# Performance work log

Hardware: AMD Instinct MI355X
Metric: run time of the kernel (lower is better)

The kernel has to match this reference:

```python
import jax, jax.numpy as jnp
import numpy as np

B, T, C, H = 4, 2048, 1024, 16


def setup_inputs() -> dict:
    key = jax.random.key(0)
    ks = jax.random.split(key, 5)
    s_attn = 1.0 / np.sqrt(C)
    s_proj = 1.0 / np.sqrt(C)
    return {
        "x": jax.random.normal(ks[0], (B, T, C), dtype=jnp.float32),
        "w_attn": jax.random.uniform(ks[1], (3 * C, C), dtype=jnp.float32, minval=-s_attn, maxval=s_attn),
        "b_attn": jax.random.uniform(ks[2], (3 * C,), dtype=jnp.float32, minval=-s_attn, maxval=s_attn),
        "w_proj": jax.random.uniform(ks[3], (C, C), dtype=jnp.float32, minval=-s_proj, maxval=s_proj),
        "b_proj": jax.random.uniform(ks[4], (C,), dtype=jnp.float32, minval=-s_proj, maxval=s_proj),
    }


def reference(x, w_attn, b_attn, w_proj, b_proj):
    b, t, c = x.shape
    hd = c // H  # head dim
    qkv = jnp.einsum('btc,dc->btd', x, w_attn) + b_attn  # [B,T,3C]
    q, k, v = jnp.split(qkv, 3, axis=-1)
    # [B,H,T,hd]
    q = q.reshape(b, t, H, hd).transpose(0, 2, 1, 3)
    k = k.reshape(b, t, H, hd).transpose(0, 2, 1, 3)
    v = v.reshape(b, t, H, hd).transpose(0, 2, 1, 3)
    att = jnp.einsum('bhqd,bhkd->bhqk', q, k) * (1.0 / np.sqrt(hd))
    mask = jnp.tril(jnp.ones((t, t), dtype=bool))  # causal
    att = jnp.where(mask, att, -jnp.inf)
    att = jax.nn.softmax(att, axis=-1)
    y = jnp.einsum('bhqk,bhkd->bhqd', att, v)
    y = y.transpose(0, 2, 1, 3).reshape(b, t, c)
    return jnp.einsum('btc,dc->btd', y, w_proj) + b_proj
```

## Files before the change

kernel.cpp:

```cpp
#include <hip/hip_runtime.h>

#define Bb 4
#define Tt 2048
#define Cc 1024
#define Hh 16
#define NQKV 3072
#define Mtot 8192

typedef __bf16 bf16_t;
typedef unsigned short u16;
typedef __bf16 bf16x8 __attribute__((ext_vector_type(8)));
typedef __bf16 bf16x4 __attribute__((ext_vector_type(4)));
typedef short short4v __attribute__((ext_vector_type(4)));
typedef float f32x4 __attribute__((ext_vector_type(4)));
typedef float f32x16 __attribute__((ext_vector_type(16)));
typedef unsigned uint2v __attribute__((ext_vector_type(2)));

union bfu { bf16_t b; u16 u; };
union trpair { short4v h[2]; bf16x8 v; };
union pfu { unsigned u[4]; bf16x8 v; };

#define QSCALE 0.18033688011112042f

#define TRD(dst, addr, OFF)                                                     \
  asm volatile("ds_read_b64_tr_b16 %0, %1 offset:" OFF                          \
               : "=v"(dst) : "v"(addr) : "memory")

__device__ __forceinline__ unsigned cvtpk(float a, float b) {
  unsigned r;
  asm("v_cvt_pk_bf16_f32 %0, %1, %2" : "=v"(r) : "v"(a), "v"(b));
  return r;
}
__device__ __forceinline__ uint2v plswap(unsigned a, unsigned b) {
  return __builtin_amdgcn_permlane32_swap(a, b, false, false);
}

__global__ __launch_bounds__(256) void cvt_f32_bf16(const float* __restrict__ s,
                                                    u16* __restrict__ d,
                                                    long nscale, float factor) {
  size_t i = ((size_t)blockIdx.x * 256 + threadIdx.x) * 8;
  const float f = ((long)i < nscale) ? factor : 1.0f;
  float4 a = *(const float4*)(s + i);
  float4 b = *(const float4*)(s + i + 4);
  bf16x8 v;
  v[0]=(bf16_t)(a.x*f); v[1]=(bf16_t)(a.y*f); v[2]=(bf16_t)(a.z*f); v[3]=(bf16_t)(a.w*f);
  v[4]=(bf16_t)(b.x*f); v[5]=(bf16_t)(b.y*f); v[6]=(bf16_t)(b.z*f); v[7]=(bf16_t)(b.w*f);
  *(bf16x8*)(d + i) = v;
}

__global__ __launch_bounds__(256) void scale_bias(const float* __restrict__ s,
                                                  float* __restrict__ d) {
  int i = blockIdx.x * 256 + threadIdx.x;
  d[i] = s[i] * ((i < Cc) ? QSCALE : 1.0f);
}

template <int OUTBF16>
__global__ __launch_bounds__(256) void gemm_bf16(
    const u16* __restrict__ A, const u16* __restrict__ Bm,
    const float* __restrict__ bias, void* __restrict__ Cout,
    int M, int N, int K)
{
  __shared__ __attribute__((aligned(16))) u16 sa[128][40];
  __shared__ __attribute__((aligned(16))) u16 sb[128][40];

  const int tid  = threadIdx.x;
  const int lane = tid & 63;
  const int wid  = tid >> 6;
  const int wr   = (wid >> 1) * 64;
  const int wc   = (wid & 1) * 64;
  const int l15  = lane & 15;
  const int lh   = lane >> 4;
  const int bm   = blockIdx.x * 128;
  const int bn   = blockIdx.y * 128;

  f32x4 acc[4][4] = {};

  const int srow = tid >> 1;
  const int sseg = (tid & 1) * 16;

  const u16* pa = A  + (size_t)(bm + srow) * K + sseg;
  const u16* pb = Bm + (size_t)(bn + srow) * K + sseg;

  uint4 ar0 = *(const uint4*)pa, ar1 = *(const uint4*)(pa + 8);
  uint4 br0 = *(const uint4*)pb, br1 = *(const uint4*)(pb + 8);
  pa += 32; pb += 32;

  for (int k0 = 0; k0 < K; k0 += 32) {
    __syncthreads();
    *(uint4*)&sa[srow][sseg]     = ar0;
    *(uint4*)&sa[srow][sseg + 8] = ar1;
    *(uint4*)&sb[srow][sseg]     = br0;
    *(uint4*)&sb[srow][sseg + 8] = br1;
    __syncthreads();
    if (k0 + 32 < K) {
      ar0 = *(const uint4*)pa; ar1 = *(const uint4*)(pa + 8);
      br0 = *(const uint4*)pb; br1 = *(const uint4*)(pb + 8);
      pa += 32; pb += 32;
    }
    bf16x8 af[4], bfv[4];
#pragma unroll
    for (int mi = 0; mi < 4; mi++)
      af[mi] = *(const bf16x8*)&sa[wr + mi*16 + l15][lh * 8];
#pragma unroll
    for (int ni = 0; ni < 4; ni++)
      bfv[ni] = *(const bf16x8*)&sb[wc + ni*16 + l15][lh * 8];
#pragma unroll
    for (int mi = 0; mi < 4; mi++)
#pragma unroll
      for (int ni = 0; ni < 4; ni++)
        acc[mi][ni] = __builtin_amdgcn_mfma_f32_16x16x32_bf16(
            af[mi], bfv[ni], acc[mi][ni], 0, 0, 0);
  }

#pragma unroll
  for (int mi = 0; mi < 4; mi++) {
#pragma unroll
    for (int ni = 0; ni < 4; ni++) {
      const int col = bn + wc + ni*16 + l15;
      const float bs = bias[col];
#pragma unroll
      for (int r = 0; r < 4; r++) {
        const int row = bm + wr + mi*16 + lh*4 + r;
        const float val = acc[mi][ni][r] + bs;
        if (OUTBF16) {
          bfu cv; cv.b = (bf16_t)val;
          ((u16*)Cout)[(size_t)row * N + col] = cv.u;
        } else {
          ((float*)Cout)[(size_t)row * N + col] = val;
        }
      }
    }
  }
}

#define V0u 4608
__global__ __launch_bounds__(256) void attn_kernel(
    const u16* __restrict__ qkv, u16* __restrict__ y)
{
  __shared__ __attribute__((aligned(16))) u16 smem[9216];

  const int tid  = threadIdx.x;
  const int lane = tid & 63;
  const int w    = tid >> 6;
  const int l31  = lane & 31;
  const int hh   = lane >> 5;
  const int l15  = lane & 15;
  const int lh   = lane >> 4;
  const int bh   = blockIdx.y;
  const int b    = bh >> 4;
  const int head = bh & 15;

  const size_t rowbase = (size_t)b * Tt * NQKV;

  const int skey = tid >> 2;
  const int sp   = tid & 3;
  const u16* kbase = qkv + rowbase + 1024 + head*64 + sp*16;
  const u16* vbase = qkv + rowbase + 2048 + head*64 + sp*16;

  const unsigned smemB = (unsigned)(size_t)(&smem[0]);
  const unsigned vaddr = smemB + 2*V0u
      + ((lh>>1)*8 + (l15>>2))*144 + (lh&1)*32 + (l15&3)*8;

  for (int half = 0; half < 2; ++half) {
    const int qb    = half ? (15 - (int)blockIdx.x) : (int)blockIdx.x;
    const int qbase = qb * 128;
    const int qw    = qbase + w * 32;
    const int qi    = qw + l31;
    const int ktiles = 2*qb + 2;

    bf16x8 qfrag[4];
#pragma unroll
    for (int m = 0; m < 4; ++m)
      qfrag[m] = *(const bf16x8*)(qkv + rowbase + (size_t)qi * NQKV
                                  + head*64 + m*16 + hh*8);

    f32x16 o0 = {}, o1 = {};
    float m_run = -1e30f, l_part = 0.0f;

    uint4 kr0 = *(const uint4*)(kbase + (size_t)skey * NQKV);
    uint4 kr1 = *(const uint4*)(kbase + (size_t)skey * NQKV + 8);
    uint4 vr0 = *(const uint4*)(vbase + (size_t)skey * NQKV);
    uint4 vr1 = *(const uint4*)(vbase + (size_t)skey * NQKV + 8);

    for (int kt = 0; kt < ktiles; ++kt) {
      __syncthreads();
      *(uint4*)&smem[skey*72 + sp*16]           = kr0;
      *(uint4*)&smem[skey*72 + sp*16 + 8]       = kr1;
      *(uint4*)&smem[V0u + skey*72 + sp*16]     = vr0;
      *(uint4*)&smem[V0u + skey*72 + sp*16 + 8] = vr1;
      __syncthreads();

      if (kt + 1 < ktiles) {
        const u16* kp = kbase + (size_t)((kt+1)*64 + skey) * NQKV;
        const u16* vp = vbase + (size_t)((kt+1)*64 + skey) * NQKV;
        kr0 = *(const uint4*)kp; kr1 = *(const uint4*)(kp + 8);
        vr0 = *(const uint4*)vp; vr1 = *(const uint4*)(vp + 8);
      }

      if (kt*64 <= qw + 31) {
        f32x16 s0 = {}, s1 = {};
#pragma unroll
        for (int m = 0; m < 4; ++m) {
          bf16x8 k0 = *(const bf16x8*)&smem[(l31)*72      + m*16 + hh*8];
          bf16x8 k1 = *(const bf16x8*)&smem[(32 + l31)*72 + m*16 + hh*8];
          s0 = __builtin_amdgcn_mfma_f32_32x32x16_bf16(k0, qfrag[m], s0, 0,0,0);
          s1 = __builtin_amdgcn_mfma_f32_32x32x16_bf16(k1, qfrag[m], s1, 0,0,0);
        }

        if (kt*64 + 63 > qw) {
          const int kb0 = kt*64;
#pragma unroll
          for (int r = 0; r < 16; ++r) {
            const int crow = (r&3) + 8*(r>>2) + 4*hh;
            if (kb0 + crow > qi)      s0[r] = -1e30f;
            if (kb0 + 32 + crow > qi) s1[r] = -1e30f;
          }
        }

        float rm = s0[0];
#pragma unroll
        for (int r = 1; r < 16; ++r) rm = fmaxf(rm, s0[r]);
#pragma unroll
        for (int r = 0; r < 16; ++r) rm = fmaxf(rm, s1[r]);
        {
          uint2v t = plswap(__float_as_uint(rm), __float_as_uint(rm));
          rm = fmaxf(__uint_as_float(t[0]), __uint_as_float(t[1]));
        }
        if (__any(rm > m_run + 8.0f)) {
          const float mn = fmaxf(m_run, rm);
          const float al = exp2f(m_run - mn);
          m_run = mn; l_part *= al;
#pragma unroll
          for (int r = 0; r < 16; ++r) { o0[r] *= al; o1[r] *= al; }
        }

        pfu pf0, pf1, pf2, pf3;
        {
          float pe[16];
#pragma unroll
          for (int r = 0; r < 16; ++r) { pe[r] = exp2f(s0[r] - m_run); l_part += pe[r]; }
          unsigned a0 = cvtpk(pe[0],pe[1]),  a1 = cvtpk(pe[2],pe[3]);
          unsigned a2 = cvtpk(pe[4],pe[5]),  a3 = cvtpk(pe[6],pe[7]);
          uint2v x1 = plswap(a0, a2), x2 = plswap(a1, a3);
          pf0.u[0]=x1[0]; pf0.u[1]=x2[0]; pf0.u[2]=x1[1]; pf0.u[3]=x2[1];
          unsigned b0 = cvtpk(pe[8],pe[9]),  b1 = cvtpk(pe[10],pe[11]);
          unsigned b2 = cvtpk(pe[12],pe[13]), b3 = cvtpk(pe[14],pe[15]);
          uint2v x3 = plswap(b0, b2), x4 = plswap(b1, b3);
          pf1.u[0]=x3[0]; pf1.u[1]=x4[0]; pf1.u[2]=x3[1]; pf1.u[3]=x4[1];
        }
        {
          float pe[16];
#pragma unroll
          for (int r = 0; r < 16; ++r) { pe[r] = exp2f(s1[r] - m_run); l_part += pe[r]; }
          unsigned a0 = cvtpk(pe[0],pe[1]),  a1 = cvtpk(pe[2],pe[3]);
          unsigned a2 = cvtpk(pe[4],pe[5]),  a3 = cvtpk(pe[6],pe[7]);
          uint2v x1 = plswap(a0, a2), x2 = plswap(a1, a3);
          pf2.u[0]=x1[0]; pf2.u[1]=x2[0]; pf2.u[2]=x1[1]; pf2.u[3]=x2[1];
          unsigned b0 = cvtpk(pe[8],pe[9]),  b1 = cvtpk(pe[10],pe[11]);
          unsigned b2 = cvtpk(pe[12],pe[13]), b3 = cvtpk(pe[14],pe[15]);
          uint2v x3 = plswap(b0, b2), x4 = plswap(b1, b3);
          pf3.u[0]=x3[0]; pf3.u[1]=x4[0]; pf3.u[2]=x3[1]; pf3.u[3]=x4[1];
        }

        short4v ta0,tb0,ta1,tb1,ta2,tb2,ta3,tb3,ta4,tb4,ta5,tb5,ta6,tb6,ta7,tb7;
        TRD(ta0, vaddr, "0");    TRD(tb0, vaddr, "576");
        TRD(ta1, vaddr, "64");   TRD(tb1, vaddr, "640");
        TRD(ta2, vaddr, "2304"); TRD(tb2, vaddr, "2880");
        TRD(ta3, vaddr, "2368"); TRD(tb3, vaddr, "2944");
        TRD(ta4, vaddr, "4608"); TRD(tb4, vaddr, "5184");
        TRD(ta5, vaddr, "4672"); TRD(tb5, vaddr, "5248");
        TRD(ta6, vaddr, "6912"); TRD(tb6, vaddr, "7488");
        TRD(ta7, vaddr, "6976"); TRD(tb7, vaddr, "7552");
        asm volatile("s_waitcnt lgkmcnt(0)" ::: "memory");
        __builtin_amdgcn_sched_barrier(0);
        trpair v00,v01,v10,v11,v20,v21,v30,v31;
        v00.h[0]=ta0; v00.h[1]=tb0;  v01.h[0]=ta1; v01.h[1]=tb1;
        v10.h[0]=ta2; v10.h[1]=tb2;  v11.h[0]=ta3; v11.h[1]=tb3;
        v20.h[0]=ta4; v20.h[1]=tb4;  v21.h[0]=ta5; v21.h[1]=tb5;
        v30.h[0]=ta6; v30.h[1]=tb6;  v31.h[0]=ta7; v31.h[1]=tb7;
        o0 = __builtin_amdgcn_mfma_f32_32x32x16_bf16(v00.v, pf0.v, o0, 0,0,0);
        o1 = __builtin_amdgcn_mfma_f32_32x32x16_bf16(v01.v, pf0.v, o1, 0,0,0);
        o0 = __builtin_amdgcn_mfma_f32_32x32x16_bf16(v10.v, pf1.v, o0, 0,0,0);
        o1 = __builtin_amdgcn_mfma_f32_32x32x16_bf16(v11.v, pf1.v, o1, 0,0,0);
        o0 = __builtin_amdgcn_mfma_f32_32x32x16_bf16(v20.v, pf2.v, o0, 0,0,0);
        o1 = __builtin_amdgcn_mfma_f32_32x32x16_bf16(v21.v, pf2.v, o1, 0,0,0);
        o0 = __builtin_amdgcn_mfma_f32_32x32x16_bf16(v30.v, pf3.v, o0, 0,0,0);
        o1 = __builtin_amdgcn_mfma_f32_32x32x16_bf16(v31.v, pf3.v, o1, 0,0,0);
      }
    }

    {
      uint2v t = plswap(__float_as_uint(l_part), __float_as_uint(l_part));
      l_part = __uint_as_float(t[0]) + __uint_as_float(t[1]);
    }
    const float inv = 1.0f / l_part;

    __syncthreads();
#pragma unroll
    for (int k4 = 0; k4 < 4; ++k4) {
      bf16x4 pa, pb;
#pragma unroll
      for (int j = 0; j < 4; ++j) {
        pa[j] = (bf16_t)(o0[4*k4 + j] * inv);
        pb[j] = (bf16_t)(o1[4*k4 + j] * inv);
      }
      *(bf16x4*)&smem[w*2304 + l31*72 +      8*k4 + 4*hh] = pa;
      *(bf16x4*)&smem[w*2304 + l31*72 + 32 + 8*k4 + 4*hh] = pb;
    }
    u16* yp = y + ((size_t)(b*Tt + qi)) * Cc + head*64;
#pragma unroll
    for (int p = 0; p < 4; ++p) {
      bf16x8 row = *(const bf16x8*)&smem[w*2304 + l31*72 + p*16 + hh*8];
      *(bf16x8*)(yp + p*16 + hh*8) = row;
    }
  }
}

extern "C" void kernel_launch(void* const* d_in, const int* in_sizes, int n_in,
                              void* d_out, int out_size, void* d_ws, size_t ws_size,
                              hipStream_t stream) {
  const float* x      = (const float*)d_in[0];
  const float* w_attn = (const float*)d_in[1];
  const float* b_attn = (const float*)d_in[2];
  const float* w_proj = (const float*)d_in[3];
  const float* b_proj = (const float*)d_in[4];
  float* out = (float*)d_out;

  char* ws = (char*)d_ws;
  u16*   xb    = (u16*)(ws + 0);
  u16*   wab   = (u16*)(ws + 16777216);
  u16*   wpb   = (u16*)(ws + 23068672);
  u16*   qkvb  = (u16*)(ws + 25165824);
  u16*   yb    = (u16*)(ws + 75497472);
  float* sbias = (float*)(ws + 92274688);

  cvt_f32_bf16<<<4096, 256, 0, stream>>>(x,      xb,  0, 1.0f);
  cvt_f32_bf16<<<1536, 256, 0, stream>>>(w_attn, wab, (long)Cc*Cc, QSCALE);
  cvt_f32_bf16<<<512,  256, 0, stream>>>(w_proj, wpb, 0, 1.0f);
  scale_bias<<<12, 256, 0, stream>>>(b_attn, sbias);

  gemm_bf16<1><<<dim3(Mtot/128, NQKV/128), 256, 0, stream>>>(
      xb, wab, sbias, (void*)qkvb, Mtot, NQKV, Cc);

  attn_kernel<<<dim3(8, Bb*Hh), 256, 0, stream>>>(qkvb, yb);

  gemm_bf16<0><<<dim3(Mtot/128, Cc/128), 256, 0, stream>>>(
      yb, wpb, b_proj, (void*)out, Mtot, Cc, Cc);
}
```

Before: 192.3 us.

## Use direct global-to-LDS loads in GEMM and split attention into one q-block per workgroup

The GEMM's tile staging changes from register-held prefetch plus LDS stores to global_load_lds direct copies into an unpadded 32-column LDS layout. This drops the register round trip, but it also drops the register-level prefetch overlap and the row padding, so LDS bank conflicts may rise. The attention kernel no longer pairs two query blocks (qb and 15-qb) per workgroup. It launches 16 workgroups per head, each handling a single q-block in reverse order so the heaviest blocks start first, which adds parallelism at the cost of less balanced per-workgroup work.

```diff
diff --git a/kernel.cpp b/kernel.cpp
--- a/kernel.cpp
+++ b/kernel.cpp
@@ -34,6 +34,11 @@
 __device__ __forceinline__ uint2v plswap(unsigned a, unsigned b) {
   return __builtin_amdgcn_permlane32_swap(a, b, false, false);
 }
+
+#define GLOAD16(gsrc, ldst)                                                     \
+  __builtin_amdgcn_global_load_lds(                                             \
+      (const __attribute__((address_space(1))) unsigned int*)(gsrc),            \
+      (__attribute__((address_space(3))) unsigned int*)(ldst), 16, 0, 0)
 
 __global__ __launch_bounds__(256) void cvt_f32_bf16(const float* __restrict__ s,
                                                     u16* __restrict__ d,
@@ -60,8 +65,8 @@
     const float* __restrict__ bias, void* __restrict__ Cout,
     int M, int N, int K)
 {
-  __shared__ __attribute__((aligned(16))) u16 sa[128][40];
-  __shared__ __attribute__((aligned(16))) u16 sb[128][40];
+  __shared__ __attribute__((aligned(16))) u16 sa[128 * 32];
+  __shared__ __attribute__((aligned(16))) u16 sb[128 * 32];
 
   const int tid  = threadIdx.x;
   const int lane = tid & 63;
@@ -75,35 +80,32 @@
 
   f32x4 acc[4][4] = {};
 
-  const int srow = tid >> 1;
-  const int sseg = (tid & 1) * 16;
-
-  const u16* pa = A  + (size_t)(bm + srow) * K + sseg;
-  const u16* pb = Bm + (size_t)(bn + srow) * K + sseg;
-
-  uint4 ar0 = *(const uint4*)pa, ar1 = *(const uint4*)(pa + 8);
-  uint4 br0 = *(const uint4*)pb, br1 = *(const uint4*)(pb + 8);
-  pa += 32; pb += 32;
+  const int r0 = wid * 32 + (lane >> 2);
+  const int c0 = (lane & 3) * 8;
+  const u16* pa0 = A  + (size_t)(bm + r0) * K + c0;
+  const u16* pb0 = Bm + (size_t)(bn + r0) * K + c0;
+  u16* sA0 = sa + wid * 1024;
+  u16* sA1 = sa + wid * 1024 + 512;
+  u16* sB0 = sb + wid * 1024;
+  u16* sB1 = sb + wid * 1024 + 512;
+  const size_t k16 = (size_t)16 * K;
 
   for (int k0 = 0; k0 < K; k0 += 32) {
     __syncthreads();
-    *(uint4*)&sa[srow][sseg]     = ar0;
-    *(uint4*)&sa[srow][sseg + 8] = ar1;
-    *(uint4*)&sb[srow][sseg]     = br0;
-    *(uint4*)&sb[srow][sseg + 8] = br1;
+    GLOAD16(pa0,       sA0);
+    GLOAD16(pa0 + k16, sA1);
+    GLOAD16(pb0,       sB0);
+    GLOAD16(pb0 + k16, sB1);
+    pa0 += 32; pb0 += 32;
     __syncthreads();
-    if (k0 + 32 < K) {
-      ar0 = *(const uint4*)pa; ar1 = *(const uint4*)(pa + 8);
-      br0 = *(const uint4*)pb; br1 = *(const uint4*)(pb + 8);
-      pa += 32; pb += 32;
-    }
+
     bf16x8 af[4], bfv[4];
 #pragma unroll
     for (int mi = 0; mi < 4; mi++)
-      af[mi] = *(const bf16x8*)&sa[wr + mi*16 + l15][lh * 8];
+      af[mi] = *(const bf16x8*)&sa[(wr + mi*16 + l15) * 32 + lh * 8];
 #pragma unroll
     for (int ni = 0; ni < 4; ni++)
-      bfv[ni] = *(const bf16x8*)&sb[wc + ni*16 + l15][lh * 8];
+      bfv[ni] = *(const bf16x8*)&sb[(wc + ni*16 + l15) * 32 + lh * 8];
 #pragma unroll
     for (int mi = 0; mi < 4; mi++)
 #pragma unroll
@@ -161,158 +163,156 @@
   const unsigned vaddr = smemB + 2*V0u
       + ((lh>>1)*8 + (l15>>2))*144 + (lh&1)*32 + (l15&3)*8;
 
-  for (int half = 0; half < 2; ++half) {
-    const int qb    = half ? (15 - (int)blockIdx.x) : (int)blockIdx.x;
-    const int qbase = qb * 128;
-    const int qw    = qbase + w * 32;
-    const int qi    = qw + l31;
-    const int ktiles = 2*qb + 2;
-
-    bf16x8 qfrag[4];
-#pragma unroll
-    for (int m = 0; m < 4; ++m)
-      qfrag[m] = *(const bf16x8*)(qkv + rowbase + (size_t)qi * NQKV
-                                  + head*64 + m*16 + hh*8);
-
-    f32x16 o0 = {}, o1 = {};
-    float m_run = -1e30f, l_part = 0.0f;
-
-    uint4 kr0 = *(const uint4*)(kbase + (size_t)skey * NQKV);
-    uint4 kr1 = *(const uint4*)(kbase + (size_t)skey * NQKV + 8);
-    uint4 vr0 = *(const uint4*)(vbase + (size_t)skey * NQKV);
-    uint4 vr1 = *(const uint4*)(vbase + (size_t)skey * NQKV + 8);
-
-    for (int kt = 0; kt < ktiles; ++kt) {
-      __syncthreads();
-      *(uint4*)&smem[skey*72 + sp*16]           = kr0;
-      *(uint4*)&smem[skey*72 + sp*16 + 8]       = kr1;
-      *(uint4*)&smem[V0u + skey*72 + sp*16]     = vr0;
-      *(uint4*)&smem[V0u + skey*72 + sp*16 + 8] = vr1;
-      __syncthreads();
-
-      if (kt + 1 < ktiles) {
-        const u16* kp = kbase + (size_t)((kt+1)*64 + skey) * NQKV;
-        const u16* vp = vbase + (size_t)((kt+1)*64 + skey) * NQKV;
-        kr0 = *(const uint4*)kp; kr1 = *(const uint4*)(kp + 8);
-        vr0 = *(const uint4*)vp; vr1 = *(const uint4*)(vp + 8);
-      }
-
-      if (kt*64 <= qw + 31) {
-        f32x16 s0 = {}, s1 = {};
-#pragma unroll
-        for (int m = 0; m < 4; ++m) {
-          bf16x8 k0 = *(const bf16x8*)&smem[(l31)*72      + m*16 + hh*8];
-          bf16x8 k1 = *(const bf16x8*)&smem[(32 + l31)*72 + m*16 + hh*8];
-          s0 = __builtin_amdgcn_mfma_f32_32x32x16_bf16(k0, qfrag[m], s0, 0,0,0);
-          s1 = __builtin_amdgcn_mfma_f32_32x32x16_bf16(k1, qfrag[m], s1, 0,0,0);
+  const int qb    = 15 - (int)blockIdx.x;
+  const int qbase = qb * 128;
+  const int qw    = qbase + w * 32;
+  const int qi    = qw + l31;
+  const int ktiles = 2*qb + 2;
+
+  bf16x8 qfrag[4];
+#pragma unroll
+  for (int m = 0; m < 4; ++m)
+    qfrag[m] = *(const bf16x8*)(qkv + rowbase + (size_t)qi * NQKV
+                                + head*64 + m*16 + hh*8);
+
+  f32x16 o0 = {}, o1 = {};
+  float m_run = -1e30f, l_part = 0.0f;
+
+  uint4 kr0 = *(const uint4*)(kbase + (size_t)skey * NQKV);
+  uint4 kr1 = *(const uint4*)(kbase + (size_t)skey * NQKV + 8);
+  uint4 vr0 = *(const uint4*)(vbase + (size_t)skey * NQKV);
+  uint4 vr1 = *(const uint4*)(vbase + (size_t)skey * NQKV + 8);
+
+  for (int kt = 0; kt < ktiles; ++kt) {
+    __syncthreads();
+    *(uint4*)&smem[skey*72 + sp*16]           = kr0;
+    *(uint4*)&smem[skey*72 + sp*16 + 8]       = kr1;
+    *(uint4*)&smem[V0u + skey*72 + sp*16]     = vr0;
+    *(uint4*)&smem[V0u + skey*72 + sp*16 + 8] = vr1;
+    __syncthreads();
+
+    if (kt + 1 < ktiles) {
+      const u16* kp = kbase + (size_t)((kt+1)*64 + skey) * NQKV;
+      const u16* vp = vbase + (size_t)((kt+1)*64 + skey) * NQKV;
+      kr0 = *(const uint4*)kp; kr1 = *(const uint4*)(kp + 8);
+      vr0 = *(const uint4*)vp; vr1 = *(const uint4*)(vp + 8);
+    }
+
+    if (kt*64 <= qw + 31) {
+      f32x16 s0 = {}, s1 = {};
+#pragma unroll
+      for (int m = 0; m < 4; ++m) {
+        bf16x8 k0 = *(const bf16x8*)&smem[(l31)*72      + m*16 + hh*8];
+        bf16x8 k1 = *(const bf16x8*)&smem[(32 + l31)*72 + m*16 + hh*8];
+        s0 = __builtin_amdgcn_mfma_f32_32x32x16_bf16(k0, qfrag[m], s0, 0,0,0);
+        s1 = __builtin_amdgcn_mfma_f32_32x32x16_bf16(k1, qfrag[m], s1, 0,0,0);
+      }
+
+      if (kt*64 + 63 > qw) {
+        const int kb0 = kt*64;
+#pragma unroll
+        for (int r = 0; r < 16; ++r) {
+          const int crow = (r&3) + 8*(r>>2) + 4*hh;
+          if (kb0 + crow > qi)      s0[r] = -1e30f;
+          if (kb0 + 32 + crow > qi) s1[r] = -1e30f;
         }
-
-        if (kt*64 + 63 > qw) {
-          const int kb0 = kt*64;
-#pragma unroll
-          for (int r = 0; r < 16; ++r) {
-            const int crow = (r&3) + 8*(r>>2) + 4*hh;
-            if (kb0 + crow > qi)      s0[r] = -1e30f;
-            if (kb0 + 32 + crow > qi) s1[r] = -1e30f;
-          }
-        }
-
-        float rm = s0[0];
-#pragma unroll
-        for (int r = 1; r < 16; ++r) rm = fmaxf(rm, s0[r]);
-#pragma unroll
-        for (int r = 0; r < 16; ++r) rm = fmaxf(rm, s1[r]);
-        {
-          uint2v t = plswap(__float_as_uint(rm), __float_as_uint(rm));
-          rm = fmaxf(__uint_as_float(t[0]), __uint_as_float(t[1]));
-        }
-        if (__any(rm > m_run + 8.0f)) {
-          const float mn = fmaxf(m_run, rm);
-          const float al = exp2f(m_run - mn);
-          m_run = mn; l_part *= al;
-#pragma unroll
-          for (int r = 0; r < 16; ++r) { o0[r] *= al; o1[r] *= al; }
-        }
-
-        pfu pf0, pf1, pf2, pf3;
-        {
-          float pe[16];
-#pragma unroll
-          for (int r = 0; r < 16; ++r) { pe[r] = exp2f(s0[r] - m_run); l_part += pe[r]; }
-          unsigned a0 = cvtpk(pe[0],pe[1]),  a1 = cvtpk(pe[2],pe[3]);
-          unsigned a2 = cvtpk(pe[4],pe[5]),  a3 = cvtpk(pe[6],pe[7]);
-          uint2v x1 = plswap(a0, a2), x2 = plswap(a1, a3);
-          pf0.u[0]=x1[0]; pf0.u[1]=x2[0]; pf0.u[2]=x1[1]; pf0.u[3]=x2[1];
-          unsigned b0 = cvtpk(pe[8],pe[9]),  b1 = cvtpk(pe[10],pe[11]);
-          unsigned b2 = cvtpk(pe[12],pe[13]), b3 = cvtpk(pe[14],pe[15]);
-          uint2v x3 = plswap(b0, b2), x4 = plswap(b1, b3);
-          pf1.u[0]=x3[0]; pf1.u[1]=x4[0]; pf1.u[2]=x3[1]; pf1.u[3]=x4[1];
-        }
-        {
-          float pe[16];
-#pragma unroll
-          for (int r = 0; r < 16; ++r) { pe[r] = exp2f(s1[r] - m_run); l_part += pe[r]; }
-          unsigned a0 = cvtpk(pe[0],pe[1]),  a1 = cvtpk(pe[2],pe[3]);
-          unsigned a2 = cvtpk(pe[4],pe[5]),  a3 = cvtpk(pe[6],pe[7]);
-          uint2v x1 = plswap(a0, a2), x2 = plswap(a1, a3);
-          pf2.u[0]=x1[0]; pf2.u[1]=x2[0]; pf2.u[2]=x1[1]; pf2.u[3]=x2[1];
-          unsigned b0 = cvtpk(pe[8],pe[9]),  b1 = cvtpk(pe[10],pe[11]);
-          unsigned b2 = cvtpk(pe[12],pe[13]), b3 = cvtpk(pe[14],pe[15]);
-          uint2v x3 = plswap(b0, b2), x4 = plswap(b1, b3);
-          pf3.u[0]=x3[0]; pf3.u[1]=x4[0]; pf3.u[2]=x3[1]; pf3.u[3]=x4[1];
-        }
-
-        short4v ta0,tb0,ta1,tb1,ta2,tb2,ta3,tb3,ta4,tb4,ta5,tb5,ta6,tb6,ta7,tb7;
-        TRD(ta0, vaddr, "0");    TRD(tb0, vaddr, "576");
-        TRD(ta1, vaddr, "64");   TRD(tb1, vaddr, "640");
-        TRD(ta2, vaddr, "2304"); TRD(tb2, vaddr, "2880");
-        TRD(ta3, vaddr, "2368"); TRD(tb3, vaddr, "2944");
-        TRD(ta4, vaddr, "4608"); TRD(tb4, vaddr, "5184");
-        TRD(ta5, vaddr, "4672"); TRD(tb5, vaddr, "5248");
-        TRD(ta6, vaddr, "6912"); TRD(tb6, vaddr, "7488");
-        TRD(ta7, vaddr, "6976"); TRD(tb7, vaddr, "7552");
-        asm volatile("s_waitcnt lgkmcnt(0)" ::: "memory");
-        __builtin_amdgcn_sched_barrier(0);
-        trpair v00,v01,v10,v11,v20,v21,v30,v31;
-        v00.h[0]=ta0; v00.h[1]=tb0;  v01.h[0]=ta1; v01.h[1]=tb1;
-        v10.h[0]=ta2; v10.h[1]=tb2;  v11.h[0]=ta3; v11.h[1]=tb3;
-        v20.h[0]=ta4; v20.h[1]=tb4;  v21.h[0]=ta5; v21.h[1]=tb5;
-        v30.h[0]=ta6; v30.h[1]=tb6;  v31.h[0]=ta7; v31.h[1]=tb7;
-        o0 = __builtin_amdgcn_mfma_f32_32x32x16_bf16(v00.v, pf0.v, o0, 0,0,0);
-        o1 = __builtin_amdgcn_mfma_f32_32x32x16_bf16(v01.v, pf0.v, o1, 0,0,0);
-        o0 = __builtin_amdgcn_mfma_f32_32x32x16_bf16(v10.v, pf1.v, o0, 0,0,0);
-        o1 = __builtin_amdgcn_mfma_f32_32x32x16_bf16(v11.v, pf1.v, o1, 0,0,0);
-        o0 = __builtin_amdgcn_mfma_f32_32x32x16_bf16(v20.v, pf2.v, o0, 0,0,0);
-        o1 = __builtin_amdgcn_mfma_f32_32x32x16_bf16(v21.v, pf2.v, o1, 0,0,0);
-        o0 = __builtin_amdgcn_mfma_f32_32x32x16_bf16(v30.v, pf3.v, o0, 0,0,0);
-        o1 = __builtin_amdgcn_mfma_f32_32x32x16_bf16(v31.v, pf3.v, o1, 0,0,0);
-      }
+      }
+
+      float rm = s0[0];
+#pragma unroll
+      for (int r = 1; r < 16; ++r) rm = fmaxf(rm, s0[r]);
+#pragma unroll
+      for (int r = 0; r < 16; ++r) rm = fmaxf(rm, s1[r]);
+      {
+        uint2v t = plswap(__float_as_uint(rm), __float_as_uint(rm));
+        rm = fmaxf(__uint_as_float(t[0]), __uint_as_float(t[1]));
+      }
+      if (__any(rm > m_run + 8.0f)) {
+        const float mn = fmaxf(m_run, rm);
+        const float al = exp2f(m_run - mn);
+        m_run = mn; l_part *= al;
+#pragma unroll
+        for (int r = 0; r < 16; ++r) { o0[r] *= al; o1[r] *= al; }
+      }
+
+      pfu pf0, pf1, pf2, pf3;
+      {
+        float pe[16];
+#pragma unroll
+        for (int r = 0; r < 16; ++r) { pe[r] = exp2f(s0[r] - m_run); l_part += pe[r]; }
+        unsigned a0 = cvtpk(pe[0],pe[1]),  a1 = cvtpk(pe[2],pe[3]);
+        unsigned a2 = cvtpk(pe[4],pe[5]),  a3 = cvtpk(pe[6],pe[7]);
+        uint2v x1 = plswap(a0, a2), x2 = plswap(a1, a3);
+        pf0.u[0]=x1[0]; pf0.u[1]=x2[0]; pf0.u[2]=x1[1]; pf0.u[3]=x2[1];
+        unsigned b0 = cvtpk(pe[8],pe[9]),  b1 = cvtpk(pe[10],pe[11]);
+        unsigned b2 = cvtpk(pe[12],pe[13]), b3 = cvtpk(pe[14],pe[15]);
+        uint2v x3 = plswap(b0, b2), x4 = plswap(b1, b3);
+        pf1.u[0]=x3[0]; pf1.u[1]=x4[0]; pf1.u[2]=x3[1]; pf1.u[3]=x4[1];
+      }
+      {
+        float pe[16];
+#pragma unroll
+        for (int r = 0; r < 16; ++r) { pe[r] = exp2f(s1[r] - m_run); l_part += pe[r]; }
+        unsigned a0 = cvtpk(pe[0],pe[1]),  a1 = cvtpk(pe[2],pe[3]);
+        unsigned a2 = cvtpk(pe[4],pe[5]),  a3 = cvtpk(pe[6],pe[7]);
+        uint2v x1 = plswap(a0, a2), x2 = plswap(a1, a3);
+        pf2.u[0]=x1[0]; pf2.u[1]=x2[0]; pf2.u[2]=x1[1]; pf2.u[3]=x2[1];
+        unsigned b0 = cvtpk(pe[8],pe[9]),  b1 = cvtpk(pe[10],pe[11]);
+        unsigned b2 = cvtpk(pe[12],pe[13]), b3 = cvtpk(pe[14],pe[15]);
+        uint2v x3 = plswap(b0, b2), x4 = plswap(b1, b3);
+        pf3.u[0]=x3[0]; pf3.u[1]=x4[0]; pf3.u[2]=x3[1]; pf3.u[3]=x4[1];
+      }
+
+      short4v ta0,tb0,ta1,tb1,ta2,tb2,ta3,tb3,ta4,tb4,ta5,tb5,ta6,tb6,ta7,tb7;
+      TRD(ta0, vaddr, "0");    TRD(tb0, vaddr, "576");
+      TRD(ta1, vaddr, "64");   TRD(tb1, vaddr, "640");
+      TRD(ta2, vaddr, "2304"); TRD(tb2, vaddr, "2880");
+      TRD(ta3, vaddr, "2368"); TRD(tb3, vaddr, "2944");
+      TRD(ta4, vaddr, "4608"); TRD(tb4, vaddr, "5184");
+      TRD(ta5, vaddr, "4672"); TRD(tb5, vaddr, "5248");
+      TRD(ta6, vaddr, "6912"); TRD(tb6, vaddr, "7488");
+      TRD(ta7, vaddr, "6976"); TRD(tb7, vaddr, "7552");
+      asm volatile("s_waitcnt lgkmcnt(0)" ::: "memory");
+      __builtin_amdgcn_sched_barrier(0);
+      trpair v00,v01,v10,v11,v20,v21,v30,v31;
+      v00.h[0]=ta0; v00.h[1]=tb0;  v01.h[0]=ta1; v01.h[1]=tb1;
+      v10.h[0]=ta2; v10.h[1]=tb2;  v11.h[0]=ta3; v11.h[1]=tb3;
+      v20.h[0]=ta4; v20.h[1]=tb4;  v21.h[0]=ta5; v21.h[1]=tb5;
+      v30.h[0]=ta6; v30.h[1]=tb6;  v31.h[0]=ta7; v31.h[1]=tb7;
+      o0 = __builtin_amdgcn_mfma_f32_32x32x16_bf16(v00.v, pf0.v, o0, 0,0,0);
+      o1 = __builtin_amdgcn_mfma_f32_32x32x16_bf16(v01.v, pf0.v, o1, 0,0,0);
+      o0 = __builtin_amdgcn_mfma_f32_32x32x16_bf16(v10.v, pf1.v, o0, 0,0,0);
+      o1 = __builtin_amdgcn_mfma_f32_32x32x16_bf16(v11.v, pf1.v, o1, 0,0,0);
+      o0 = __builtin_amdgcn_mfma_f32_32x32x16_bf16(v20.v, pf2.v, o0, 0,0,0);
+      o1 = __builtin_amdgcn_mfma_f32_32x32x16_bf16(v21.v, pf2.v, o1, 0,0,0);
+      o0 = __builtin_amdgcn_mfma_f32_32x32x16_bf16(v30.v, pf3.v, o0, 0,0,0);
+      o1 = __builtin_amdgcn_mfma_f32_32x32x16_bf16(v31.v, pf3.v, o1, 0,0,0);
     }
-
-    {
-      uint2v t = plswap(__float_as_uint(l_part), __float_as_uint(l_part));
-      l_part = __uint_as_float(t[0]) + __uint_as_float(t[1]);
+  }
+
+  {
+    uint2v t = plswap(__float_as_uint(l_part), __float_as_uint(l_part));
+    l_part = __uint_as_float(t[0]) + __uint_as_float(t[1]);
+  }
+  const float inv = 1.0f / l_part;
+
+  __syncthreads();
+#pragma unroll
+  for (int k4 = 0; k4 < 4; ++k4) {
+    bf16x4 pa, pb;
+#pragma unroll
+    for (int j = 0; j < 4; ++j) {
+      pa[j] = (bf16_t)(o0[4*k4 + j] * inv);
+      pb[j] = (bf16_t)(o1[4*k4 + j] * inv);
     }
-    const float inv = 1.0f / l_part;
-
-    __syncthreads();
-#pragma unroll
-    for (int k4 = 0; k4 < 4; ++k4) {
-      bf16x4 pa, pb;
-#pragma unroll
-      for (int j = 0; j < 4; ++j) {
-        pa[j] = (bf16_t)(o0[4*k4 + j] * inv);
-        pb[j] = (bf16_t)(o1[4*k4 + j] * inv);
-      }
-      *(bf16x4*)&smem[w*2304 + l31*72 +      8*k4 + 4*hh] = pa;
-      *(bf16x4*)&smem[w*2304 + l31*72 + 32 + 8*k4 + 4*hh] = pb;
-    }
-    u16* yp = y + ((size_t)(b*Tt + qi)) * Cc + head*64;
-#pragma unroll
-    for (int p = 0; p < 4; ++p) {
-      bf16x8 row = *(const bf16x8*)&smem[w*2304 + l31*72 + p*16 + hh*8];
-      *(bf16x8*)(yp + p*16 + hh*8) = row;
-    }
+    *(bf16x4*)&smem[w*2304 + l31*72 +      8*k4 + 4*hh] = pa;
+    *(bf16x4*)&smem[w*2304 + l31*72 + 32 + 8*k4 + 4*hh] = pb;
+  }
+  u16* yp = y + ((size_t)(b*Tt + qi)) * Cc + head*64;
+#pragma unroll
+  for (int p = 0; p < 4; ++p) {
+    bf16x8 row = *(const bf16x8*)&smem[w*2304 + l31*72 + p*16 + hh*8];
+    *(bf16x8*)(yp + p*16 + hh*8) = row;
   }
 }
 
@@ -342,7 +342,7 @@
   gemm_bf16<1><<<dim3(Mtot/128, NQKV/128), 256, 0, stream>>>(
       xb, wab, sbias, (void*)qkvb, Mtot, NQKV, Cc);
 
-  attn_kernel<<<dim3(8, Bb*Hh), 256, 0, stream>>>(qkvb, yb);
+  attn_kernel<<<dim3(16, Bb*Hh), 256, 0, stream>>>(qkvb, yb);
 
   gemm_bf16<0><<<dim3(Mtot/128, Cc/128), 256, 0, stream>>>(
       yb, wpb, b_proj, (void*)out, Mtot, Cc, Cc);
```

After: 249.8 us. 1.3x slower.

## Double attention key tile to 128 keys and pipeline PV in sections

Applied to the files above, without the earlier changes.

The attention kernel now stages 128 keys per iteration instead of 64, with shared memory doubled and each thread loading 32-element K/V chunks. This halves the number of block-wide barriers and global-to-shared staging rounds per query block, and the row-max reduction becomes a tree. The PV product is split into four macro sections, each interleaving its transposed V loads with the exp/convert work for one score block, so LDS reads overlap ALU work. The cost is more registers and LDS, lower occupancy, and more work wasted on masked keys: the per-warp causal skip is gone, so waves whose rows lie entirely before the tile's upper half still compute it.

```diff
diff --git a/kernel.cpp b/kernel.cpp
--- a/kernel.cpp
+++ b/kernel.cpp
@@ -133,11 +133,42 @@
   }
 }
 
-#define V0u 4608
+#define VBYTE 18432
+
+#define PVSEC(SV, A0,A1,A2,A3, A4,A5,A6,A7) do {                                \
+  short4v t0,t1,t2,t3,t4,t5,t6,t7;                                              \
+  TRD(t0, vaddr, A0); TRD(t1, vaddr, A1); TRD(t2, vaddr, A2);                   \
+  TRD(t3, vaddr, A3); TRD(t4, vaddr, A4); TRD(t5, vaddr, A5);                   \
+  TRD(t6, vaddr, A6); TRD(t7, vaddr, A7);                                       \
+  pfu pfa, pfb;                                                                 \
+  {                                                                             \
+    float pe[16];                                                               \
+    _Pragma("unroll")                                                           \
+    for (int r = 0; r < 16; ++r) { pe[r] = exp2f(SV[r] - m_run); l_part += pe[r]; } \
+    unsigned a0=cvtpk(pe[0],pe[1]),   a1=cvtpk(pe[2],pe[3]);                    \
+    unsigned a2=cvtpk(pe[4],pe[5]),   a3=cvtpk(pe[6],pe[7]);                    \
+    uint2v x1=plswap(a0,a2), x2=plswap(a1,a3);                                  \
+    pfa.u[0]=x1[0]; pfa.u[1]=x2[0]; pfa.u[2]=x1[1]; pfa.u[3]=x2[1];             \
+    unsigned b0=cvtpk(pe[8],pe[9]),   b1=cvtpk(pe[10],pe[11]);                  \
+    unsigned b2=cvtpk(pe[12],pe[13]), b3=cvtpk(pe[14],pe[15]);                  \
+    uint2v x3=plswap(b0,b2), x4=plswap(b1,b3);                                  \
+    pfb.u[0]=x3[0]; pfb.u[1]=x4[0]; pfb.u[2]=x3[1]; pfb.u[3]=x4[1];             \
+  }                                                                             \
+  asm volatile("s_waitcnt lgkmcnt(0)" ::: "memory");                            \
+  __builtin_amdgcn_sched_barrier(0);                                            \
+  trpair va,vb,vc,vd;                                                           \
+  va.h[0]=t0; va.h[1]=t1;  vb.h[0]=t2; vb.h[1]=t3;                              \
+  vc.h[0]=t4; vc.h[1]=t5;  vd.h[0]=t6; vd.h[1]=t7;                              \
+  o0 = __builtin_amdgcn_mfma_f32_32x32x16_bf16(va.v, pfa.v, o0, 0,0,0);         \
+  o1 = __builtin_amdgcn_mfma_f32_32x32x16_bf16(vb.v, pfa.v, o1, 0,0,0);         \
+  o0 = __builtin_amdgcn_mfma_f32_32x32x16_bf16(vc.v, pfb.v, o0, 0,0,0);         \
+  o1 = __builtin_amdgcn_mfma_f32_32x32x16_bf16(vd.v, pfb.v, o1, 0,0,0);         \
+} while (0)
+
 __global__ __launch_bounds__(256) void attn_kernel(
     const u16* __restrict__ qkv, u16* __restrict__ y)
 {
-  __shared__ __attribute__((aligned(16))) u16 smem[9216];
+  __shared__ __attribute__((aligned(16))) u16 smem[18432];
 
   const int tid  = threadIdx.x;
   const int lane = tid & 63;
@@ -152,13 +183,13 @@
 
   const size_t rowbase = (size_t)b * Tt * NQKV;
 
-  const int skey = tid >> 2;
-  const int sp   = tid & 3;
-  const u16* kbase = qkv + rowbase + 1024 + head*64 + sp*16;
-  const u16* vbase = qkv + rowbase + 2048 + head*64 + sp*16;
+  const int skey = tid >> 1;
+  const int sp   = tid & 1;
+  const u16* kbase = qkv + rowbase + 1024 + head*64 + sp*32;
+  const u16* vbase = qkv + rowbase + 2048 + head*64 + sp*32;
 
   const unsigned smemB = (unsigned)(size_t)(&smem[0]);
-  const unsigned vaddr = smemB + 2*V0u
+  const unsigned vaddr = smemB + VBYTE
       + ((lh>>1)*8 + (l15>>2))*144 + (lh&1)*32 + (l15&3)*8;
 
   for (int half = 0; half < 2; ++half) {
@@ -166,7 +197,7 @@
     const int qbase = qb * 128;
     const int qw    = qbase + w * 32;
     const int qi    = qw + l31;
-    const int ktiles = 2*qb + 2;
+    const int ktiles = qb + 1;
 
     bf16x8 qfrag[4];
 #pragma unroll
@@ -177,116 +208,90 @@
     f32x16 o0 = {}, o1 = {};
     float m_run = -1e30f, l_part = 0.0f;
 
-    uint4 kr0 = *(const uint4*)(kbase + (size_t)skey * NQKV);
-    uint4 kr1 = *(const uint4*)(kbase + (size_t)skey * NQKV + 8);
-    uint4 vr0 = *(const uint4*)(vbase + (size_t)skey * NQKV);
-    uint4 vr1 = *(const uint4*)(vbase + (size_t)skey * NQKV + 8);
+    uint4 kr0, kr1, kr2, kr3, vr0, vr1, vr2, vr3;
+    {
+      const u16* kp = kbase + (size_t)skey * NQKV;
+      const u16* vp = vbase + (size_t)skey * NQKV;
+      kr0 = ((const uint4*)kp)[0]; kr1 = ((const uint4*)kp)[1];
+      kr2 = ((const uint4*)kp)[2]; kr3 = ((const uint4*)kp)[3];
+      vr0 = ((const uint4*)vp)[0]; vr1 = ((const uint4*)vp)[1];
+      vr2 = ((const uint4*)vp)[2]; vr3 = ((const uint4*)vp)[3];
+    }
 
     for (int kt = 0; kt < ktiles; ++kt) {
       __syncthreads();
-      *(uint4*)&smem[skey*72 + sp*16]           = kr0;
-      *(uint4*)&smem[skey*72 + sp*16 + 8]       = kr1;
-      *(uint4*)&smem[V0u + skey*72 + sp*16]     = vr0;
-      *(uint4*)&smem[V0u + skey*72 + sp*16 + 8] = vr1;
+      {
+        u16* dK = &smem[skey*72 + sp*32];
+        *(uint4*)dK        = kr0; *(uint4*)(dK + 8)  = kr1;
+        *(uint4*)(dK + 16) = kr2; *(uint4*)(dK + 24) = kr3;
+        u16* dV = dK + 9216;
+        *(uint4*)dV        = vr0; *(uint4*)(dV + 8)  = vr1;
+        *(uint4*)(dV + 16) = vr2; *(uint4*)(dV + 24) = vr3;
+      }
       __syncthreads();
 
       if (kt + 1 < ktiles) {
-        const u16* kp = kbase + (size_t)((kt+1)*64 + skey) * NQKV;
-        const u16* vp = vbase + (size_t)((kt+1)*64 + skey) * NQKV;
-        kr0 = *(const uint4*)kp; kr1 = *(const uint4*)(kp + 8);
-        vr0 = *(const uint4*)vp; vr1 = *(const uint4*)(vp + 8);
-      }
-
-      if (kt*64 <= qw + 31) {
-        f32x16 s0 = {}, s1 = {};
-#pragma unroll
-        for (int m = 0; m < 4; ++m) {
-          bf16x8 k0 = *(const bf16x8*)&smem[(l31)*72      + m*16 + hh*8];
-          bf16x8 k1 = *(const bf16x8*)&smem[(32 + l31)*72 + m*16 + hh*8];
-          s0 = __builtin_amdgcn_mfma_f32_32x32x16_bf16(k0, qfrag[m], s0, 0,0,0);
-          s1 = __builtin_amdgcn_mfma_f32_32x32x16_bf16(k1, qfrag[m], s1, 0,0,0);
+        const u16* kp = kbase + (size_t)((kt+1)*128 + skey) * NQKV;
+        const u16* vp = vbase + (size_t)((kt+1)*128 + skey) * NQKV;
+        kr0 = ((const uint4*)kp)[0]; kr1 = ((const uint4*)kp)[1];
+        kr2 = ((const uint4*)kp)[2]; kr3 = ((const uint4*)kp)[3];
+        vr0 = ((const uint4*)vp)[0]; vr1 = ((const uint4*)vp)[1];
+        vr2 = ((const uint4*)vp)[2]; vr3 = ((const uint4*)vp)[3];
+      }
+
+      f32x16 s0 = {}, s1 = {}, s2 = {}, s3 = {};
+#pragma unroll
+      for (int m = 0; m < 4; ++m) {
+        const int co = m*16 + hh*8;
+        bf16x8 k0 = *(const bf16x8*)&smem[(l31)*72      + co];
+        bf16x8 k1 = *(const bf16x8*)&smem[(32 + l31)*72 + co];
+        bf16x8 k2 = *(const bf16x8*)&smem[(64 + l31)*72 + co];
+        bf16x8 k3 = *(const bf16x8*)&smem[(96 + l31)*72 + co];
+        s0 = __builtin_amdgcn_mfma_f32_32x32x16_bf16(k0, qfrag[m], s0, 0,0,0);
+        s1 = __builtin_amdgcn_mfma_f32_32x32x16_bf16(k1, qfrag[m], s1, 0,0,0);
+        s2 = __builtin_amdgcn_mfma_f32_32x32x16_bf16(k2, qfrag[m], s2, 0,0,0);
+        s3 = __builtin_amdgcn_mfma_f32_32x32x16_bf16(k3, qfrag[m], s3, 0,0,0);
+      }
+
+      if (kt*128 + 127 > qw) {
+        const int kb0 = kt*128;
+#pragma unroll
+        for (int r = 0; r < 16; ++r) {
+          const int crow = (r&3) + 8*(r>>2) + 4*hh;
+          if (kb0 + crow > qi)      s0[r] = -1e30f;
+          if (kb0 + 32 + crow > qi) s1[r] = -1e30f;
+          if (kb0 + 64 + crow > qi) s2[r] = -1e30f;
+          if (kb0 + 96 + crow > qi) s3[r] = -1e30f;
         }
-
-        if (kt*64 + 63 > qw) {
-          const int kb0 = kt*64;
-#pragma unroll
-          for (int r = 0; r < 16; ++r) {
-            const int crow = (r&3) + 8*(r>>2) + 4*hh;
-            if (kb0 + crow > qi)      s0[r] = -1e30f;
-            if (kb0 + 32 + crow > qi) s1[r] = -1e30f;
-          }
-        }
-
-        float rm = s0[0];
-#pragma unroll
-        for (int r = 1; r < 16; ++r) rm = fmaxf(rm, s0[r]);
-#pragma unroll
-        for (int r = 0; r < 16; ++r) rm = fmaxf(rm, s1[r]);
-        {
-          uint2v t = plswap(__float_as_uint(rm), __float_as_uint(rm));
-          rm = fmaxf(__uint_as_float(t[0]), __uint_as_float(t[1]));
-        }
-        if (__any(rm > m_run + 8.0f)) {
-          const float mn = fmaxf(m_run, rm);
-          const float al = exp2f(m_run - mn);
-          m_run = mn; l_part *= al;
-#pragma unroll
-          for (int r = 0; r < 16; ++r) { o0[r] *= al; o1[r] *= al; }
-        }
-
-        pfu pf0, pf1, pf2, pf3;
-        {
-          float pe[16];
-#pragma unroll
-          for (int r = 0; r < 16; ++r) { pe[r] = exp2f(s0[r] - m_run); l_part += pe[r]; }
-          unsigned a0 = cvtpk(pe[0],pe[1]),  a1 = cvtpk(pe[2],pe[3]);
-          unsigned a2 = cvtpk(pe[4],pe[5]),  a3 = cvtpk(pe[6],pe[7]);
-          uint2v x1 = plswap(a0, a2), x2 = plswap(a1, a3);
-          pf0.u[0]=x1[0]; pf0.u[1]=x2[0]; pf0.u[2]=x1[1]; pf0.u[3]=x2[1];
-          unsigned b0 = cvtpk(pe[8],pe[9]),  b1 = cvtpk(pe[10],pe[11]);
-          unsigned b2 = cvtpk(pe[12],pe[13]), b3 = cvtpk(pe[14],pe[15]);
-          uint2v x3 = plswap(b0, b2), x4 = plswap(b1, b3);
-          pf1.u[0]=x3[0]; pf1.u[1]=x4[0]; pf1.u[2]=x3[1]; pf1.u[3]=x4[1];
-        }
-        {
-          float pe[16];
-#pragma unroll
-          for (int r = 0; r < 16; ++r) { pe[r] = exp2f(s1[r] - m_run); l_part += pe[r]; }
-          unsigned a0 = cvtpk(pe[0],pe[1]),  a1 = cvtpk(pe[2],pe[3]);
-          unsigned a2 = cvtpk(pe[4],pe[5]),  a3 = cvtpk(pe[6],pe[7]);
-          uint2v x1 = plswap(a0, a2), x2 = plswap(a1, a3);
-          pf2.u[0]=x1[0]; pf2.u[1]=x2[0]; pf2.u[2]=x1[1]; pf2.u[3]=x2[1];
-          unsigned b0 = cvtpk(pe[8],pe[9]),  b1 = cvtpk(pe[10],pe[11]);
-          unsigned b2 = cvtpk(pe[12],pe[13]), b3 = cvtpk(pe[14],pe[15]);
-          uint2v x3 = plswap(b0, b2), x4 = plswap(b1, b3);
-          pf3.u[0]=x3[0]; pf3.u[1]=x4[0]; pf3.u[2]=x3[1]; pf3.u[3]=x4[1];
-        }
-
-        short4v ta0,tb0,ta1,tb1,ta2,tb2,ta3,tb3,ta4,tb4,ta5,tb5,ta6,tb6,ta7,tb7;
-        TRD(ta0, vaddr, "0");    TRD(tb0, vaddr, "576");
-        TRD(ta1, vaddr, "64");   TRD(tb1, vaddr, "640");
-        TRD(ta2, vaddr, "2304"); TRD(tb2, vaddr, "2880");
-        TRD(ta3, vaddr, "2368"); TRD(tb3, vaddr, "2944");
-        TRD(ta4, vaddr, "4608"); TRD(tb4, vaddr, "5184");
-        TRD(ta5, vaddr, "4672"); TRD(tb5, vaddr, "5248");
-        TRD(ta6, vaddr, "6912"); TRD(tb6, vaddr, "7488");
-        TRD(ta7, vaddr, "6976"); TRD(tb7, vaddr, "7552");
-        asm volatile("s_waitcnt lgkmcnt(0)" ::: "memory");
-        __builtin_amdgcn_sched_barrier(0);
-        trpair v00,v01,v10,v11,v20,v21,v30,v31;
-        v00.h[0]=ta0; v00.h[1]=tb0;  v01.h[0]=ta1; v01.h[1]=tb1;
-        v10.h[0]=ta2; v10.h[1]=tb2;  v11.h[0]=ta3; v11.h[1]=tb3;
-        v20.h[0]=ta4; v20.h[1]=tb4;  v21.h[0]=ta5; v21.h[1]=tb5;
-        v30.h[0]=ta6; v30.h[1]=tb6;  v31.h[0]=ta7; v31.h[1]=tb7;
-        o0 = __builtin_amdgcn_mfma_f32_32x32x16_bf16(v00.v, pf0.v, o0, 0,0,0);
-        o1 = __builtin_amdgcn_mfma_f32_32x32x16_bf16(v01.v, pf0.v, o1, 0,0,0);
-        o0 = __builtin_amdgcn_mfma_f32_32x32x16_bf16(v10.v, pf1.v, o0, 0,0,0);
-        o1 = __builtin_amdgcn_mfma_f32_32x32x16_bf16(v11.v, pf1.v, o1, 0,0,0);
-        o0 = __builtin_amdgcn_mfma_f32_32x32x16_bf16(v20.v, pf2.v, o0, 0,0,0);
-        o1 = __builtin_amdgcn_mfma_f32_32x32x16_bf16(v21.v, pf2.v, o1, 0,0,0);
-        o0 = __builtin_amdgcn_mfma_f32_32x32x16_bf16(v30.v, pf3.v, o0, 0,0,0);
-        o1 = __builtin_amdgcn_mfma_f32_32x32x16_bf16(v31.v, pf3.v, o1, 0,0,0);
-      }
+      }
+
+      float ma[16];
+#pragma unroll
+      for (int r = 0; r < 16; ++r)
+        ma[r] = fmaxf(fmaxf(s0[r], s1[r]), fmaxf(s2[r], s3[r]));
+      float t8[8], t4[4], t2[2];
+#pragma unroll
+      for (int i = 0; i < 8; ++i) t8[i] = fmaxf(ma[i], ma[i+8]);
+#pragma unroll
+      for (int i = 0; i < 4; ++i) t4[i] = fmaxf(t8[i], t8[i+4]);
+      t2[0] = fmaxf(t4[0], t4[2]); t2[1] = fmaxf(t4[1], t4[3]);
+      float rm = fmaxf(t2[0], t2[1]);
+      {
+        uint2v t = plswap(__float_as_uint(rm), __float_as_uint(rm));
+        rm = fmaxf(__uint_as_float(t[0]), __uint_as_float(t[1]));
+      }
+      if (__any(rm > m_run + 8.0f)) {
+        const float mn = fmaxf(m_run, rm);
+        const float al = exp2f(m_run - mn);
+        m_run = mn; l_part *= al;
+#pragma unroll
+        for (int r = 0; r < 16; ++r) { o0[r] *= al; o1[r] *= al; }
+      }
+
+      PVSEC(s0, "0","576","64","640",          "2304","2880","2368","2944");
+      PVSEC(s1, "4608","5184","4672","5248",   "6912","7488","6976","7552");
+      PVSEC(s2, "9216","9792","9280","9856",   "11520","12096","11584","12160");
+      PVSEC(s3, "13824","14400","13888","14464","16128","16704","16192","16768");
     }
 
     {
```

Result: slower. 220.7 us (+14.8%).

## Split attention key range across two wave groups with in-block softmax merge

Applied to the files above, without the earlier changes.

The attention block grows from 256 to 512 threads. Two groups of four waves each process alternating 64-key halves of a 128-key tile for the same 128 queries, which halves the serial key-tile loop per wave. At the end, group 1 writes its running max, sum and partial O into shared memory, and group 0 merges them with the rescaled online-softmax combine before normalizing and storing. This adds parallelism per (batch, head) block and uses twice the LDS, at the cost of a merge step, extra barriers, and higher register and LDS pressure per CU.

```diff
diff --git a/kernel.cpp b/kernel.cpp
--- a/kernel.cpp
+++ b/kernel.cpp
@@ -19,6 +19,7 @@
 union bfu { bf16_t b; u16 u; };
 union trpair { short4v h[2]; bf16x8 v; };
 union pfu { unsigned u[4]; bf16x8 v; };
+union o16 { f32x16 v; f32x4 q[4]; };
 
 #define QSCALE 0.18033688011112042f
 
@@ -133,15 +134,16 @@
   }
 }
 
-#define V0u 4608
-__global__ __launch_bounds__(256) void attn_kernel(
+__global__ __launch_bounds__(512, 4) void attn_kernel(
     const u16* __restrict__ qkv, u16* __restrict__ y)
 {
-  __shared__ __attribute__((aligned(16))) u16 smem[9216];
+  __shared__ __attribute__((aligned(16))) u16 smem[18432];
 
   const int tid  = threadIdx.x;
   const int lane = tid & 63;
   const int w    = tid >> 6;
+  const int hw   = w >> 2;
+  const int ch   = w & 3;
   const int l31  = lane & 31;
   const int hh   = lane >> 5;
   const int l15  = lane & 15;
@@ -158,15 +160,15 @@
   const u16* vbase = qkv + rowbase + 2048 + head*64 + sp*16;
 
   const unsigned smemB = (unsigned)(size_t)(&smem[0]);
-  const unsigned vaddr = smemB + 2*V0u
+  const unsigned vaddr = smemB + 18432 + hw*9216
       + ((lh>>1)*8 + (l15>>2))*144 + (lh&1)*32 + (l15&3)*8;
 
   for (int half = 0; half < 2; ++half) {
     const int qb    = half ? (15 - (int)blockIdx.x) : (int)blockIdx.x;
     const int qbase = qb * 128;
-    const int qw    = qbase + w * 32;
+    const int qw    = qbase + ch * 32;
     const int qi    = qw + l31;
-    const int ktiles = 2*qb + 2;
+    const int ktiles = qb + 1;
 
     bf16x8 qfrag[4];
 #pragma unroll
@@ -177,43 +179,47 @@
     f32x16 o0 = {}, o1 = {};
     float m_run = -1e30f, l_part = 0.0f;
 
-    uint4 kr0 = *(const uint4*)(kbase + (size_t)skey * NQKV);
-    uint4 kr1 = *(const uint4*)(kbase + (size_t)skey * NQKV + 8);
-    uint4 vr0 = *(const uint4*)(vbase + (size_t)skey * NQKV);
-    uint4 vr1 = *(const uint4*)(vbase + (size_t)skey * NQKV + 8);
+    uint4 kr0, kr1, vr0, vr1;
+    {
+      const u16* kp = kbase + (size_t)skey * NQKV;
+      const u16* vp = vbase + (size_t)skey * NQKV;
+      kr0 = ((const uint4*)kp)[0]; kr1 = ((const uint4*)kp)[1];
+      vr0 = ((const uint4*)vp)[0]; vr1 = ((const uint4*)vp)[1];
+    }
 
     for (int kt = 0; kt < ktiles; ++kt) {
       __syncthreads();
-      *(uint4*)&smem[skey*72 + sp*16]           = kr0;
-      *(uint4*)&smem[skey*72 + sp*16 + 8]       = kr1;
-      *(uint4*)&smem[V0u + skey*72 + sp*16]     = vr0;
-      *(uint4*)&smem[V0u + skey*72 + sp*16 + 8] = vr1;
+      *(uint4*)&smem[skey*72 + sp*16]          = kr0;
+      *(uint4*)&smem[skey*72 + sp*16 + 8]      = kr1;
+      *(uint4*)&smem[9216 + skey*72 + sp*16]   = vr0;
+      *(uint4*)&smem[9216 + skey*72 + sp*16+8] = vr1;
       __syncthreads();
 
       if (kt + 1 < ktiles) {
-        const u16* kp = kbase + (size_t)((kt+1)*64 + skey) * NQKV;
-        const u16* vp = vbase + (size_t)((kt+1)*64 + skey) * NQKV;
-        kr0 = *(const uint4*)kp; kr1 = *(const uint4*)(kp + 8);
-        vr0 = *(const uint4*)vp; vr1 = *(const uint4*)(vp + 8);
-      }
-
-      if (kt*64 <= qw + 31) {
+        const u16* kp = kbase + (size_t)((kt+1)*128 + skey) * NQKV;
+        const u16* vp = vbase + (size_t)((kt+1)*128 + skey) * NQKV;
+        kr0 = ((const uint4*)kp)[0]; kr1 = ((const uint4*)kp)[1];
+        vr0 = ((const uint4*)vp)[0]; vr1 = ((const uint4*)vp)[1];
+      }
+
+      const int keyw = kt*128 + hw*64;
+      if (keyw <= qw + 31) {
         f32x16 s0 = {}, s1 = {};
 #pragma unroll
         for (int m = 0; m < 4; ++m) {
-          bf16x8 k0 = *(const bf16x8*)&smem[(l31)*72      + m*16 + hh*8];
-          bf16x8 k1 = *(const bf16x8*)&smem[(32 + l31)*72 + m*16 + hh*8];
+          const int co = m*16 + hh*8;
+          bf16x8 k0 = *(const bf16x8*)&smem[(hw*64 +      l31)*72 + co];
+          bf16x8 k1 = *(const bf16x8*)&smem[(hw*64 + 32 + l31)*72 + co];
           s0 = __builtin_amdgcn_mfma_f32_32x32x16_bf16(k0, qfrag[m], s0, 0,0,0);
           s1 = __builtin_amdgcn_mfma_f32_32x32x16_bf16(k1, qfrag[m], s1, 0,0,0);
         }
 
-        if (kt*64 + 63 > qw) {
-          const int kb0 = kt*64;
+        if (keyw + 63 > qw) {
 #pragma unroll
           for (int r = 0; r < 16; ++r) {
             const int crow = (r&3) + 8*(r>>2) + 4*hh;
-            if (kb0 + crow > qi)      s0[r] = -1e30f;
-            if (kb0 + 32 + crow > qi) s1[r] = -1e30f;
+            if (keyw + crow > qi)      s0[r] = -1e30f;
+            if (keyw + 32 + crow > qi) s1[r] = -1e30f;
           }
         }
 
@@ -289,29 +295,58 @@
       }
     }
 
-    {
-      uint2v t = plswap(__float_as_uint(l_part), __float_as_uint(l_part));
-      l_part = __uint_as_float(t[0]) + __uint_as_float(t[1]);
-    }
-    const float inv = 1.0f / l_part;
-
     __syncthreads();
-#pragma unroll
-    for (int k4 = 0; k4 < 4; ++k4) {
-      bf16x4 pa, pb;
-#pragma unroll
-      for (int j = 0; j < 4; ++j) {
-        pa[j] = (bf16_t)(o0[4*k4 + j] * inv);
-        pb[j] = (bf16_t)(o1[4*k4 + j] * inv);
-      }
-      *(bf16x4*)&smem[w*2304 + l31*72 +      8*k4 + 4*hh] = pa;
-      *(bf16x4*)&smem[w*2304 + l31*72 + 32 + 8*k4 + 4*hh] = pb;
-    }
-    u16* yp = y + ((size_t)(b*Tt + qi)) * Cc + head*64;
-#pragma unroll
-    for (int p = 0; p < 4; ++p) {
-      bf16x8 row = *(const bf16x8*)&smem[w*2304 + l31*72 + p*16 + hh*8];
-      *(bf16x8*)(yp + p*16 + hh*8) = row;
+    if (hw == 1) {
+      float* p = (float*)&smem[ch*4608 + lane*72];
+      p[0] = m_run; p[1] = l_part;
+      o16 ua, ub; ua.v = o0; ub.v = o1;
+#pragma unroll
+      for (int i = 0; i < 4; ++i) {
+        *(f32x4*)(p + 4  + 4*i) = ua.q[i];
+        *(f32x4*)(p + 20 + 4*i) = ub.q[i];
+      }
+    }
+    __syncthreads();
+    if (hw == 0) {
+      const float* p = (const float*)&smem[ch*4608 + lane*72];
+      const float mB = p[0], lB = p[1];
+      const float mN = fmaxf(m_run, mB);
+      const float fA = exp2f(m_run - mN), fB = exp2f(mB - mN);
+      l_part = l_part*fA + lB*fB;
+#pragma unroll
+      for (int i = 0; i < 4; ++i) {
+        f32x4 qa = *(const f32x4*)(p + 4  + 4*i);
+        f32x4 qb4 = *(const f32x4*)(p + 20 + 4*i);
+#pragma unroll
+        for (int j = 0; j < 4; ++j) {
+          o0[4*i+j] = o0[4*i+j]*fA + qa[j]*fB;
+          o1[4*i+j] = o1[4*i+j]*fA + qb4[j]*fB;
+        }
+      }
+
+      {
+        uint2v t = plswap(__float_as_uint(l_part), __float_as_uint(l_part));
+        l_part = __uint_as_float(t[0]) + __uint_as_float(t[1]);
+      }
+      const float inv = 1.0f / l_part;
+      const int scr = ch*4608 + 2304;
+#pragma unroll
+      for (int k4 = 0; k4 < 4; ++k4) {
+        bf16x4 pa, pb;
+#pragma unroll
+        for (int j = 0; j < 4; ++j) {
+          pa[j] = (bf16_t)(o0[4*k4 + j] * inv);
+          pb[j] = (bf16_t)(o1[4*k4 + j] * inv);
+        }
+        *(bf16x4*)&smem[scr + l31*72 +      8*k4 + 4*hh] = pa;
+        *(bf16x4*)&smem[scr + l31*72 + 32 + 8*k4 + 4*hh] = pb;
+      }
+      u16* yp = y + ((size_t)(b*Tt + qi)) * Cc + head*64;
+#pragma unroll
+      for (int pcol = 0; pcol < 4; ++pcol) {
+        bf16x8 row = *(const bf16x8*)&smem[scr + l31*72 + pcol*16 + hh*8];
+        *(bf16x8*)(yp + pcol*16 + hh*8) = row;
+      }
     }
   }
 }
@@ -342,7 +377,7 @@
   gemm_bf16<1><<<dim3(Mtot/128, NQKV/128), 256, 0, stream>>>(
       xb, wab, sbias, (void*)qkvb, Mtot, NQKV, Cc);
 
-  attn_kernel<<<dim3(8, Bb*Hh), 256, 0, stream>>>(qkvb, yb);
+  attn_kernel<<<dim3(8, Bb*Hh), 512, 0, stream>>>(qkvb, yb);
 
   gemm_bf16<0><<<dim3(Mtot/128, Cc/128), 256, 0, stream>>>(
       yb, wpb, b_proj, (void*)out, Mtot, Cc, Cc);
```

New measurement: 198.3 us. +3.1%, slower.
